# Performance work log

Hardware: AMD Instinct MI355X
Metric: run time of the kernel (lower is better)

The kernel has to match this reference:

```python
import jax, jax.numpy as jnp
import numpy as np

N_NODES = 50000
N_EDGES = 1600000
HID = 128
N_LAYERS = 2
N_REL = 8


def setup_inputs() -> dict:
    key = jax.random.key(0)
    ks = jax.random.split(key, 8)
    node_id = jnp.arange(N_NODES, dtype=jnp.int64 if jax.config.jax_enable_x64 else jnp.int32)
    src = jax.random.randint(ks[0], (N_EDGES,), 0, N_NODES)
    dst = jax.random.randint(ks[1], (N_EDGES,), 0, N_NODES)
    edge_type = jax.random.randint(ks[2], (N_EDGES,), 0, N_REL)
    # parameters
    emb = jax.random.normal(ks[3], (N_NODES, HID), dtype=jnp.float32) * 0.02
    # per-layer relation weights (basis regularizer with num_bases = num_rel
    # degenerates to one full weight per relation)
    W = jax.random.normal(ks[4], (N_LAYERS, N_REL, HID, HID), dtype=jnp.float32) * (1.0 / np.sqrt(HID))
    W_loop = jax.random.normal(ks[5], (N_LAYERS, HID, HID), dtype=jnp.float32) * (1.0 / np.sqrt(HID))
    bias = jnp.zeros((N_LAYERS, HID), dtype=jnp.float32)
    return {"node_id": node_id, "src": src, "dst": dst, "edge_type": edge_type,
            "emb": emb, "W": W, "W_loop": W_loop, "bias": bias}


def reference(node_id, src, dst, edge_type, emb, W, W_loop, bias):
    # h = Embedding(node_id)
    h = emb[node_id]  # [N, d]
    n = h.shape[0]
    for l in range(W.shape[0]):  # fixed small number of layers
        # transform every node by every relation once: [R, N, d]
        # (equivalent to low_mem per-relation matmuls, fully vectorized)
        X = jnp.einsum('nd,rdk->rnk', h, W[l])
        # gather per-edge message msg_e = X[etype_e, src_e] : [E, d]
        msg = X[edge_type, src]
        # scatter-add to destination nodes
        agg = jax.ops.segment_sum(msg, dst, num_segments=n)
        # self-loop + bias (DGL RelGraphConv defaults: self_loop=True,
        # bias=True, activation=None; dropout omitted = eval mode)
        h = agg + h @ W_loop[l] + bias[l]
    return h
```

## Files before the change

### kernel.cpp

```cpp
#include <hip/hip_runtime.h>
#include <stdint.h>

#define N_NODES 50000
#define N_EDGES 1600000
#define HID 128
#define NB 196
#define CHUNK 8192
#define NCH 196
#define TOT (NB * NCH)
#define NGB 6250
#define NCW 1152
#define NMB 782

typedef float f32x4 __attribute__((ext_vector_type(4)));
typedef float f32x2 __attribute__((ext_vector_type(2)));
typedef short s16x8 __attribute__((ext_vector_type(8)));
typedef unsigned u32x4 __attribute__((ext_vector_type(4)));

__device__ __forceinline__ unsigned short f2bf(float f) {
  unsigned u = __float_as_uint(f);
  u += 0x7fffu + ((u >> 16) & 1u);
  return (unsigned short)(u >> 16);
}

__device__ __forceinline__ int block_scan_excl(int v, int t) {
  const int lane = t & 63, wid = t >> 6;
  int incl = v;
  #pragma unroll
  for (int o = 1; o < 64; o <<= 1) {
    int nv = __shfl_up(incl, o);
    if (lane >= o) incl += nv;
  }
  __shared__ int wsum[4];
  if (lane == 63) wsum[wid] = incl;
  __syncthreads();
  int wbase = 0;
  #pragma unroll
  for (int w = 0; w < 3; ++w) if (w < wid) wbase += wsum[w];
  return wbase + incl - v;
}

__global__ void k_pre(const int* __restrict__ nid, const float* __restrict__ emb,
                      unsigned short* __restrict__ h0,
                      const int* __restrict__ dst, int* __restrict__ histT,
                      const float* __restrict__ W, const float* __restrict__ Wl,
                      unsigned short* __restrict__ Wt) {
  const int bid = blockIdx.x, t = threadIdx.x;
  if (bid < NGB) {
    int g = bid * 256 + t;
    int i = g >> 5, c = (g & 31) * 4;
    const float4 v = *(const float4*)(emb + (size_t)nid[i] * HID + c);
    ushort4 o;
    o.x = f2bf(v.x); o.y = f2bf(v.y); o.z = f2bf(v.z); o.w = f2bf(v.w);
    *(ushort4*)(h0 + (size_t)i * HID + c) = o;
  } else if (bid < NGB + NCH) {
    __shared__ int h[NB];
    const int c = bid - NGB;
    if (t < NB) h[t] = 0;
    __syncthreads();
    int base = c * CHUNK;
    #pragma unroll 4
    for (int i = t; i < CHUNK; i += 256) {
      int e = base + i;
      if (e < N_EDGES) atomicAdd(&h[dst[e] >> 8], 1);
    }
    __syncthreads();
    if (t < NB) histT[t * NCH + c] = h[t];
  } else {
    int idx = (bid - NGB - NCH) * 256 + t;
    int d  = idx & 127;
    int k  = (idx >> 7) & 127;
    int lr = idx >> 14;
    int l = lr / 9, r = lr - l * 9;
    float v;
    if (r < 8) v = W[((((size_t)l * 8 + r) * 128) + d) * 128 + k];
    else       v = Wl[(((size_t)l * 128) + d) * 128 + k];
    Wt[idx] = f2bf(v);
  }
}

__global__ void k_scan_buckets(const int* __restrict__ histT, int* __restrict__ curL,
                               int* __restrict__ btot) {
  const int b = blockIdx.x, tid = threadIdx.x;
  int carry = 0;
  #pragma unroll
  for (int k = 0; k < 4; ++k) {
    int c = k * 64 + tid;
    int v = (c < NCH) ? histT[b * NCH + c] : 0;
    int incl = v;
    #pragma unroll
    for (int o = 1; o < 64; o <<= 1) {
      int nv = __shfl_up(incl, o);
      if (tid >= o) incl += nv;
    }
    if (c < NCH) curL[b * NCH + c] = carry + incl - v;
    carry += __shfl(incl, 63);
  }
  if (tid == 0) btot[b] = carry;
}

__global__ void k_scan_top(const int* __restrict__ btot, int* __restrict__ bbase,
                           int* __restrict__ rowptr) {
  const int t = threadIdx.x;
  int v = (t < NB) ? btot[t] : 0;
  int ex = block_scan_excl(v, t);
  if (t < NB) bbase[t] = ex;
  if (t == 0) { bbase[NB] = N_EDGES; rowptr[N_NODES] = N_EDGES; }
}

template <bool SCAT>
__global__ __launch_bounds__(256, 5) void k_gemm9(
    const unsigned short* __restrict__ A,
    const unsigned short* __restrict__ Bw,
    unsigned short* __restrict__ X,
    const int* __restrict__ src, const int* __restrict__ dst,
    const int* __restrict__ et, const int* __restrict__ curL,
    const int* __restrict__ bbase, unsigned* __restrict__ tmp) {
  __shared__ unsigned char Ws[32768];
  const int t = threadIdx.x;
  if (SCAT && blockIdx.x >= NMB) {
    int* off2 = (int*)Ws;
    const int c = blockIdx.x - NMB;
    if (t < NB) off2[t] = curL[t * NCH + c] + bbase[t];
    __syncthreads();
    int base = c * CHUNK;
    #pragma unroll 4
    for (int i = t; i < CHUNK; i += 256) {
      int e = base + i;
      if (e < N_EDGES) {
        int d = dst[e];
        int pos = atomicAdd(&off2[d >> 8], 1);
        tmp[pos] = ((unsigned)(d & 255) << 19) | ((unsigned)et[e] << 16) | (unsigned)src[e];
      }
    }
    return;
  }
  const int mb = blockIdx.x;
  const int wid = t >> 6, lane = t & 63;
  const int lr = lane & 15, kg = (lane >> 4) * 8;
  const int rAg = mb * 64 + wid * 16 + lr;
  const bool rok = rAg < N_NODES;
  const unsigned short* Arow = A + (size_t)(rok ? rAg : 0) * 128;
  s16x8 a[4];
  #pragma unroll
  for (int kk = 0; kk < 4; ++kk) {
    s16x8 v = (s16x8)(short)0;
    if (rok) v = *(const s16x8*)(Arow + kk * 32 + kg);
    a[kk] = v;
  }
  for (int rel = 0; rel < 9; ++rel) {
    const unsigned char* Bsrc = (const unsigned char*)(Bw + (size_t)rel * 16384);
    #pragma unroll
    for (int c = 0; c < 8; ++c) {
      int off = c * 4096 + t * 16;
      int row = off >> 8, ib = off & 255;
      *(u32x4*)(Ws + row * 256 + (ib ^ ((row & 7) << 4))) = *(const u32x4*)(Bsrc + off);
    }
    __syncthreads();
    f32x4 acc[8];
    #pragma unroll
    for (int n = 0; n < 8; ++n) acc[n] = (f32x4)(0.f);
    #pragma unroll
    for (int kk = 0; kk < 4; ++kk) {
      const int kb = (kk * 32 + kg) * 2;
      #pragma unroll
      for (int n = 0; n < 8; ++n) {
        int cc = n * 16 + lr;
        s16x8 b = *(const s16x8*)(Ws + cc * 256 + (kb ^ ((cc & 7) << 4)));
        acc[n] = __builtin_amdgcn_mfma_f32_16x16x32_bf16(a[kk], b, acc[n], 0, 0, 0);
      }
    }
    const int rbase = mb * 64 + wid * 16 + (lane >> 4) * 4;
    #pragma unroll
    for (int n = 0; n < 8; ++n) {
      int col = n * 16 + lr;
      #pragma unroll
      for (int j = 0; j < 4; ++j) {
        int grow = rbase + j;
        if (grow < N_NODES)
          X[((size_t)rel * N_NODES + grow) * 128 + col] = f2bf(acc[n][j]);
      }
    }
    __syncthreads();
  }
}

__global__ void k_bucket_finalize(const unsigned* __restrict__ tmp,
                                  const int* __restrict__ bbase,
                                  int* __restrict__ rowptr,
                                  unsigned* __restrict__ keys) {
  __shared__ int cnt[256];
  __shared__ int off[256];
  const int b = blockIdx.x;
  const int t = threadIdx.x;
  const int s = bbase[b], e = bbase[b + 1];
  cnt[t] = 0;
  __syncthreads();
  for (int i = s + t; i < e; i += 256)
    atomicAdd(&cnt[(tmp[i] >> 19) & 255u], 1);
  __syncthreads();
  int ex = block_scan_excl(cnt[t], t);
  int node = b * 256 + t;
  if (node < N_NODES) rowptr[node] = s + ex;
  off[t] = s + ex;
  __syncthreads();
  for (int i = s + t; i < e; i += 256) {
    unsigned r = tmp[i];
    int pos = atomicAdd(&off[(r >> 19) & 255u], 1);
    keys[pos] = ((r >> 16) & 7u) * N_NODES + (r & 0xffffu);
  }
}

template <bool LAST>
__global__ void k_aggregate(const unsigned short* __restrict__ X,
                            const unsigned* __restrict__ keys,
                            const int* __restrict__ rowptr,
                            const float* __restrict__ bias,
                            void* __restrict__ out) {
  const int t = threadIdx.x;
  const int v = blockIdx.x * 4 + (t >> 6);
  const int lane = t & 63;
  const int start = rowptr[v], end = rowptr[v + 1];
  const unsigned char* Xb = (const unsigned char*)X;
  float a0 = 0.f, a1 = 0.f;
  int e = start;
  const int n16 = start + ((end - start) & ~15);
  for (; e < n16; e += 16) {
    unsigned kk[16], pp[16];
    #pragma unroll
    for (int q = 0; q < 16; ++q) kk[q] = keys[e + q];
    #pragma unroll
    for (int q = 0; q < 16; ++q)
      pp[q] = *(const unsigned*)(Xb + ((size_t)kk[q] << 8) + lane * 4);
    #pragma unroll
    for (int q = 0; q < 16; ++q) {
      a0 += __uint_as_float(pp[q] << 16);
      a1 += __uint_as_float(pp[q] & 0xffff0000u);
    }
  }
  const int n4 = start + ((end - start) & ~3);
  for (; e < n4; e += 4) {
    unsigned kk[4], pp[4];
    #pragma unroll
    for (int q = 0; q < 4; ++q) kk[q] = keys[e + q];
    #pragma unroll
    for (int q = 0; q < 4; ++q)
      pp[q] = *(const unsigned*)(Xb + ((size_t)kk[q] << 8) + lane * 4);
    #pragma unroll
    for (int q = 0; q < 4; ++q) {
      a0 += __uint_as_float(pp[q] << 16);
      a1 += __uint_as_float(pp[q] & 0xffff0000u);
    }
  }
  for (; e < end; ++e) {
    unsigned k0 = keys[e];
    unsigned p0 = *(const unsigned*)(Xb + ((size_t)k0 << 8) + lane * 4);
    a0 += __uint_as_float(p0 << 16); a1 += __uint_as_float(p0 & 0xffff0000u);
  }
  {
    unsigned p = *(const unsigned*)(Xb + (((size_t)8 * N_NODES + v) << 8) + lane * 4);
    a0 += __uint_as_float(p << 16); a1 += __uint_as_float(p & 0xffff0000u);
  }
  const float2 bb = *(const float2*)(bias + lane * 2);
  a0 += bb.x; a1 += bb.y;
  if (LAST) {
    f32x2 o; o.x = a0; o.y = a1;
    __builtin_nontemporal_store(o, (f32x2*)((float*)out + (size_t)v * 128 + lane * 2));
  } else {
    unsigned po = ((unsigned)f2bf(a1) << 16) | (unsigned)f2bf(a0);
    *(unsigned*)((unsigned short*)out + (size_t)v * 128 + lane * 2) = po;
  }
}

extern "C" void kernel_launch(void* const* d_in, const int* in_sizes, int n_in,
                              void* d_out, int out_size, void* d_ws, size_t ws_size,
                              hipStream_t stream) {
  const int*   nid  = (const int*)d_in[0];
  const int*   src  = (const int*)d_in[1];
  const int*   dst  = (const int*)d_in[2];
  const int*   et   = (const int*)d_in[3];
  const float* emb  = (const float*)d_in[4];
  const float* W    = (const float*)d_in[5];
  const float* Wl   = (const float*)d_in[6];
  const float* bias = (const float*)d_in[7];

  unsigned char* ws = (unsigned char*)d_ws;
  size_t off = 0;
  auto alloc = [&](size_t bytes) {
    void* p = ws + off;
    off = (off + bytes + 255) & ~(size_t)255;
    return p;
  };
  unsigned short* X    = (unsigned short*)alloc((size_t)9 * N_NODES * HID * 2);
  unsigned short* h0   = (unsigned short*)alloc((size_t)N_NODES * HID * 2);
  unsigned short* h1   = (unsigned short*)alloc((size_t)N_NODES * HID * 2);
  unsigned short* Wt   = (unsigned short*)alloc((size_t)2 * 9 * 128 * 128 * 2);
  unsigned*       keys = (unsigned*)alloc((size_t)N_EDGES * 4);
  int*            rowp = (int*)alloc((size_t)(N_NODES + 1) * 4);
  int*            histT= (int*)alloc((size_t)TOT * 4);
  int*            curL = (int*)alloc((size_t)TOT * 4);
  int*            btot = (int*)alloc((size_t)NB * 4);
  int*            bbas = (int*)alloc((size_t)(NB + 1) * 4);
  unsigned*       tmp  = (unsigned*)h1;

  k_pre<<<NGB + NCH + NCW, 256, 0, stream>>>(nid, emb, h0, dst, histT, W, Wl, Wt);
  k_scan_buckets<<<NB, 64, 0, stream>>>(histT, curL, btot);
  k_scan_top<<<1, 256, 0, stream>>>(btot, bbas, rowp);
  k_gemm9<true><<<NMB + NCH, 256, 0, stream>>>(h0, Wt, X, src, dst, et, curL, bbas, tmp);
  k_bucket_finalize<<<NB, 256, 0, stream>>>(tmp, bbas, rowp, keys);

  const int agrid = N_NODES / 4;
  k_aggregate<false><<<agrid, 256, 0, stream>>>(X, keys, rowp, bias, (void*)h1);
  k_gemm9<false><<<NMB, 256, 0, stream>>>(h1, Wt + (size_t)9 * 128 * 128, X,
                                          src, dst, et, curL, bbas, tmp);
  k_aggregate<true><<<agrid, 256, 0, stream>>>(X, keys, rowp, bias + HID, (void*)d_out);
}
```

Measured before the change: 245.4 us.

## Permute hidden-column layout so GEMM epilogue writes 16-byte packed rows

Hidden features are now kept in a permuted column order (pos2col) across the embedding copy, transposed weights, bias and intermediate X. With that order each lane's eight MFMA accumulators for a row are contiguous, so the GEMM epilogue writes one 16-byte vector per row instead of 32 scattered 2-byte stores. The final aggregate un-permutes through shared memory before the fp32 output store. The cost is strided scalar reads of the embedding in preprocessing and an extra LDS round trip plus barrier in the last aggregate.

```diff
diff --git a/kernel.cpp b/kernel.cpp
--- a/kernel.cpp
+++ b/kernel.cpp
@@ -17,6 +17,8 @@
 typedef short s16x8 __attribute__((ext_vector_type(8)));
 typedef unsigned u32x4 __attribute__((ext_vector_type(4)));
 
+__device__ __forceinline__ int pos2col(int p) { return (p & 7) * 16 + (p >> 3); }
+
 __device__ __forceinline__ unsigned short f2bf(float f) {
   unsigned u = __float_as_uint(f);
   u += 0x7fffu + ((u >> 16) & 1u);
@@ -44,15 +46,19 @@
                       unsigned short* __restrict__ h0,
                       const int* __restrict__ dst, int* __restrict__ histT,
                       const float* __restrict__ W, const float* __restrict__ Wl,
-                      unsigned short* __restrict__ Wt) {
+                      unsigned short* __restrict__ Wt,
+                      const float* __restrict__ bias, float* __restrict__ biasP) {
   const int bid = blockIdx.x, t = threadIdx.x;
   if (bid < NGB) {
     int g = bid * 256 + t;
-    int i = g >> 5, c = (g & 31) * 4;
-    const float4 v = *(const float4*)(emb + (size_t)nid[i] * HID + c);
+    int i = g >> 5, s = g & 31;
+    const float* erow = emb + (size_t)nid[i] * HID;
     ushort4 o;
-    o.x = f2bf(v.x); o.y = f2bf(v.y); o.z = f2bf(v.z); o.w = f2bf(v.w);
-    *(ushort4*)(h0 + (size_t)i * HID + c) = o;
+    o.x = f2bf(erow[pos2col(4 * s + 0)]);
+    o.y = f2bf(erow[pos2col(4 * s + 1)]);
+    o.z = f2bf(erow[pos2col(4 * s + 2)]);
+    o.w = f2bf(erow[pos2col(4 * s + 3)]);
+    *(ushort4*)(h0 + (size_t)i * HID + 4 * s) = o;
   } else if (bid < NGB + NCH) {
     __shared__ int h[NB];
     const int c = bid - NGB;
@@ -66,16 +72,20 @@
     }
     __syncthreads();
     if (t < NB) histT[t * NCH + c] = h[t];
-  } else {
+  } else if (bid < NGB + NCH + NCW) {
     int idx = (bid - NGB - NCH) * 256 + t;
-    int d  = idx & 127;
+    int p  = idx & 127;
     int k  = (idx >> 7) & 127;
     int lr = idx >> 14;
     int l = lr / 9, r = lr - l * 9;
+    int d = pos2col(p);
     float v;
     if (r < 8) v = W[((((size_t)l * 8 + r) * 128) + d) * 128 + k];
     else       v = Wl[(((size_t)l * 128) + d) * 128 + k];
     Wt[idx] = f2bf(v);
+  } else {
+    int l = t >> 7, p = t & 127;
+    biasP[t] = bias[l * 128 + pos2col(p)];
   }
 }
 
@@ -170,15 +180,16 @@
         acc[n] = __builtin_amdgcn_mfma_f32_16x16x32_bf16(a[kk], b, acc[n], 0, 0, 0);
       }
     }
-    const int rbase = mb * 64 + wid * 16 + (lane >> 4) * 4;
-    #pragma unroll
-    for (int n = 0; n < 8; ++n) {
-      int col = n * 16 + lr;
-      #pragma unroll
-      for (int j = 0; j < 4; ++j) {
-        int grow = rbase + j;
-        if (grow < N_NODES)
-          X[((size_t)rel * N_NODES + grow) * 128 + col] = f2bf(acc[n][j]);
+    #pragma unroll
+    for (int j = 0; j < 4; ++j) {
+      int grow = mb * 64 + wid * 16 + (lane >> 4) * 4 + j;
+      if (grow < N_NODES) {
+        u32x4 pk;
+        pk.x = (unsigned)f2bf(acc[0][j]) | ((unsigned)f2bf(acc[1][j]) << 16);
+        pk.y = (unsigned)f2bf(acc[2][j]) | ((unsigned)f2bf(acc[3][j]) << 16);
+        pk.z = (unsigned)f2bf(acc[4][j]) | ((unsigned)f2bf(acc[5][j]) << 16);
+        pk.w = (unsigned)f2bf(acc[6][j]) | ((unsigned)f2bf(acc[7][j]) << 16);
+        *(u32x4*)((unsigned char*)X + ((size_t)rel * N_NODES + grow) * 256 + lr * 16) = pk;
       }
     }
     __syncthreads();
@@ -215,10 +226,12 @@
 __global__ void k_aggregate(const unsigned short* __restrict__ X,
                             const unsigned* __restrict__ keys,
                             const int* __restrict__ rowptr,
-                            const float* __restrict__ bias,
+                            const float* __restrict__ biasP,
                             void* __restrict__ out) {
+  __shared__ float ob[4][128];
   const int t = threadIdx.x;
-  const int v = blockIdx.x * 4 + (t >> 6);
+  const int w = t >> 6;
+  const int v = blockIdx.x * 4 + w;
   const int lane = t & 63;
   const int start = rowptr[v], end = rowptr[v + 1];
   const unsigned char* Xb = (const unsigned char*)X;
@@ -261,10 +274,14 @@
     unsigned p = *(const unsigned*)(Xb + (((size_t)8 * N_NODES + v) << 8) + lane * 4);
     a0 += __uint_as_float(p << 16); a1 += __uint_as_float(p & 0xffff0000u);
   }
-  const float2 bb = *(const float2*)(bias + lane * 2);
+  const float2 bb = *(const float2*)(biasP + lane * 2);
   a0 += bb.x; a1 += bb.y;
   if (LAST) {
-    f32x2 o; o.x = a0; o.y = a1;
+    int c0 = ((2 * lane) & 7) * 16 + (lane >> 2);
+    ob[w][c0] = a0;
+    ob[w][c0 + 16] = a1;
+    __syncthreads();
+    f32x2 o = *(const f32x2*)&ob[w][lane * 2];
     __builtin_nontemporal_store(o, (f32x2*)((float*)out + (size_t)v * 128 + lane * 2));
   } else {
     unsigned po = ((unsigned)f2bf(a1) << 16) | (unsigned)f2bf(a0);
@@ -301,17 +318,19 @@
   int*            curL = (int*)alloc((size_t)TOT * 4);
   int*            btot = (int*)alloc((size_t)NB * 4);
   int*            bbas = (int*)alloc((size_t)(NB + 1) * 4);
+  float*          biasP= (float*)alloc((size_t)2 * 128 * 4);
   unsigned*       tmp  = (unsigned*)h1;
 
-  k_pre<<<NGB + NCH + NCW, 256, 0, stream>>>(nid, emb, h0, dst, histT, W, Wl, Wt);
+  k_pre<<<NGB + NCH + NCW + 1, 256, 0, stream>>>(nid, emb, h0, dst, histT, W, Wl, Wt,
+                                                 bias, biasP);
   k_scan_buckets<<<NB, 64, 0, stream>>>(histT, curL, btot);
   k_scan_top<<<1, 256, 0, stream>>>(btot, bbas, rowp);
   k_gemm9<true><<<NMB + NCH, 256, 0, stream>>>(h0, Wt, X, src, dst, et, curL, bbas, tmp);
   k_bucket_finalize<<<NB, 256, 0, stream>>>(tmp, bbas, rowp, keys);
 
   const int agrid = N_NODES / 4;
-  k_aggregate<false><<<agrid, 256, 0, stream>>>(X, keys, rowp, bias, (void*)h1);
+  k_aggregate<false><<<agrid, 256, 0, stream>>>(X, keys, rowp, biasP, (void*)h1);
   k_gemm9<false><<<NMB, 256, 0, stream>>>(h1, Wt + (size_t)9 * 128 * 128, X,
                                           src, dst, et, curL, bbas, tmp);
-  k_aggregate<true><<<agrid, 256, 0, stream>>>(X, keys, rowp, bias + HID, (void*)d_out);
-}
+  k_aggregate<true><<<agrid, 256, 0, stream>>>(X, keys, rowp, biasP + HID, (void*)d_out);
+}
```

After: 243.5 us. Within noise of the previous version (-0.7%).
